# Kernel tuning notes

Hardware: AMD Instinct MI355X
Metric: run time of the kernel (lower is better)

The kernel has to match this reference:

```python
import math
import numpy as np
import jax
import jax.numpy as jnp

B_IN, B_L1, B_L2 = 10, 6, 3
BATCH, NUM_POINTS = 4, 512
F1, F2, F_OUT = 8, 16, 10
NB = BATCH * NUM_POINTS
N_GRID_S2, N_GRID_SO3 = 24, 144


def _lf(n):
    return math.lgamma(n + 1)


def wigner_d(l, beta):
    """Wigner small-d matrices d^l_{m',m}(beta). beta: np [K] -> [K, 2l+1, 2l+1]."""
    beta = np.asarray(beta, dtype=np.float64)
    K = beta.shape[0]
    d = np.zeros((K, 2 * l + 1, 2 * l + 1))
    c, s = np.cos(beta / 2.0), np.sin(beta / 2.0)
    for mi, mp in enumerate(range(-l, l + 1)):
        for ni, m in enumerate(range(-l, l + 1)):
            k0, k1 = max(0, m - mp), min(l + m, l - mp)
            acc = np.zeros(K)
            for k in range(k0, k1 + 1):
                lg = 0.5 * (_lf(l + mp) + _lf(l - mp) + _lf(l + m) + _lf(l - m)) - _lf(l + m - k) - _lf(k) - _lf(mp - m + k) - _lf(l - mp - k)
                acc = acc + ((-1.0) ** (mp - m + k)) * np.exp(lg) * c ** (2 * l - 2 * k + m - mp) * s ** (mp - m + 2 * k)
            d[:, mi, ni] = acc
    return d


def quad_beta_weights(b):
    """Driscoll-Healy quadrature betas and weights at bandwidth b."""
    k = np.arange(2 * b)
    beta = np.pi * (2 * k + 1) / (4 * b)
    j = np.arange(b)[:, None]
    w = (2.0 / b) * np.sin(beta) * np.sum(np.sin((2 * j + 1) * beta[None, :]) / (2 * j + 1), axis=0)
    return beta, w


# near-identity kernel grids (as in s2cnn): s2 grid 3 betas x 8 alphas, so3 grid x 6 gammas
_b = np.arange(1, 4) * (np.pi / 8) / 3
_a = np.linspace(0, 2 * np.pi, 8, endpoint=False)
_GB1, _GA1 = [g.ravel() for g in np.meshgrid(_b, _a, indexing='ij')]
_g = np.linspace(0, 2 * np.pi, 6, endpoint=False)
_GB2, _GA2, _GG2 = [g.ravel() for g in np.meshgrid(_b, _a, _g, indexing='ij')]

_BETA_IN, _W_IN = quad_beta_weights(B_IN)
_BETA_L1, _W_L1 = quad_beta_weights(B_L1)
_BETA_L2, _W_L2 = quad_beta_weights(B_L2)

# S2 FFT tables: quadrature-weighted d^l_{m,0}(beta_k), l < b_l1
_S2FFT_D = [jnp.asarray((wigner_d(l, _BETA_IN)[:, :, l] * _W_IN[:, None]).astype(np.complex64)) for l in range(B_L1)]
# S2 kernel basis psi1[l]: [24, 2l+1] = d^l_{m,0}(beta_g) e^{-i m alpha_g}
_PSI1 = []
for l in range(B_L1):
    m = np.arange(-l, l + 1)
    _PSI1.append(jnp.asarray((wigner_d(l, _GB1)[:, :, l] * np.exp(-1j * m[None, :] * _GA1[:, None])).astype(np.complex64)))
# SO3 inverse-FFT d matrices at b_l1 quadrature betas
_D_L1 = [jnp.asarray(wigner_d(l, _BETA_L1).astype(np.complex64)) for l in range(B_L1)]
# SO3 FFT tables at b_l1 (output bandwidth b_l2)
_SO3FFT_D = [jnp.asarray((wigner_d(l, _BETA_L1) * _W_L1[:, None, None]).astype(np.complex64)) for l in range(B_L2)]
# SO3 kernel basis psi2[l]: [144, 2l+1, 2l+1] = e^{-i m a} d^l_{mn}(b) e^{-i n g}
_PSI2 = []
for l in range(B_L2):
    m = np.arange(-l, l + 1)
    ph = np.exp(-1j * m[None, :, None] * _GA2[:, None, None]) * np.exp(-1j * m[None, None, :] * _GG2[:, None, None])
    _PSI2.append(jnp.asarray((wigner_d(l, _GB2) * ph).astype(np.complex64)))
_D_L2 = [jnp.asarray(wigner_d(l, _BETA_L2).astype(np.complex64)) for l in range(B_L2)]
_W_INT = jnp.asarray(_W_L2.astype(np.float32))


def s2_fft(x, b_out):
    # x: [n, f, 2b(beta), 2b(alpha)] real -> list_l of [n, f, 2l+1] complex
    two_b = x.shape[-1]
    F = jnp.fft.fft(x, axis=-1)
    out = []
    for l in range(b_out):
        idx = np.arange(-l, l + 1) % two_b
        out.append(jnp.einsum('nfkm,km->nfm', F[..., idx], _S2FFT_D[l]))
    return out


def so3_ifft_list(z, b_out, d_list):
    # z[l]: [n, fo, 2l+1(m), 2l+1(p)] -> real [n, fo, 2b(beta), 2b(alpha), 2b(gamma)]
    n2 = 2 * b_out
    n, fo = z[0].shape[:2]
    Fh = jnp.zeros((n, fo, n2, n2, n2), jnp.complex64)
    for l in range(b_out):
        idx = np.arange(-l, l + 1) % n2
        blk = (2 * l + 1) * jnp.einsum('nomp,kmp->nokmp', z[l], d_list[l])
        Fh = Fh.at[:, :, :, idx[:, None], idx[None, :]].add(blk)
    return jnp.real(jnp.fft.ifft2(Fh, axes=(-2, -1)) * (n2 * n2))


def s2_conv(x, w, bias):
    xs = s2_fft(x, B_L1)
    wc = w.astype(jnp.complex64)
    z = []
    for l in range(B_L1):
        y = jnp.einsum('iog,gm->iom', wc, _PSI1[l])  # kernel spectrum [fi, fo, 2l+1]
        z.append(jnp.einsum('nim,iop->nomp', xs[l], jnp.conj(y)))
    return so3_ifft_list(z, B_L1, _D_L1) + bias[None, :, None, None, None]


def so3_fft(x, b_out):
    # x: [n, f, 2b(beta), 2b(alpha), 2b(gamma)] -> list_l of [n, f, 2l+1, 2l+1]
    two_b = x.shape[-1]
    F = jnp.fft.fft2(x, axes=(-2, -1))
    out = []
    for l in range(b_out):
        idx = np.arange(-l, l + 1) % two_b
        out.append(jnp.einsum('nfkmp,kmp->nfmp', F[:, :, :, idx[:, None], idx[None, :]], _SO3FFT_D[l]))
    return out


def so3_conv(x, w, bias):
    xs = so3_fft(x, B_L2)
    wc = w.astype(jnp.complex64)
    z = []
    for l in range(B_L2):
        y = jnp.einsum('iog,gmp->iomp', wc, _PSI2[l])  # [fi, fo, 2l+1, 2l+1]
        z.append(jnp.einsum('nimk,iopk->nomp', xs[l], jnp.conj(y)))
    return so3_ifft_list(z, B_L2, _D_L2) + bias[None, :, None, None, None]


def so3_integrate(x):
    # mean over alpha, gamma; quadrature-weighted sum over beta
    return jnp.einsum('nfk,k->nf', x.mean(axis=(-2, -1)), _W_INT)


def forward(x, w1, b1, w2, b2, w_out, bias_out):
    h = jax.nn.relu(s2_conv(x, w1, b1))
    h = jax.nn.relu(so3_conv(h, w2, b2))
    feat = so3_integrate(h).reshape(BATCH, NUM_POINTS, F2).transpose(0, 2, 1)  # [B, F2, P]
    pooled = feat.max(axis=-1)  # MaxPool1d(kernel_size=num_points) + squeeze
    return pooled @ w_out.T + bias_out


def setup_inputs():
    ks = jax.random.split(jax.random.key(0), 4)
    return {
        'x': jax.random.normal(ks[0], (NB, 1, 2 * B_IN, 2 * B_IN), jnp.float32),
        'w1': jax.random.normal(ks[1], (1, F1, N_GRID_S2), jnp.float32) * 0.1,
        'b1': jnp.zeros((F1,), jnp.float32),
        'w2': jax.random.normal(ks[2], (F1, F2, N_GRID_SO3), jnp.float32) * 0.05,
        'b2': jnp.zeros((F2,), jnp.float32),
        'w_out': jax.random.normal(ks[3], (F_OUT, F2), jnp.float32) * 0.1,
        'bias_out': jnp.zeros((F_OUT,), jnp.float32),
    }


def reference(x, w1, b1, w2, b2, w_out, bias_out):
    return forward(x, w1, b1, w2, b2, w_out, bias_out)
```

## Files before the change

### kernel.cpp

```cpp
#include <hip/hip_runtime.h>
#include <cmath>

typedef float2 c32;

__device__ __forceinline__ void cmadd(c32& acc, c32 a, float cr, float ci){
    acc.x += a.x*cr - a.y*ci;
    acc.y += a.x*ci + a.y*cr;
}

__host__ __device__ constexpr int M12(int x){ return ((x%12)+12)%12; }
__host__ __device__ constexpr int M6(int x){ return ((x%6)+6)%6; }

#define SQ32 0.86602540378443864676f
#define RT22 0.70710678118654752440f
static constexpr float CW12[12] = {1.f, SQ32, 0.5f, 0.f, -0.5f, -SQ32, -1.f, -SQ32, -0.5f, 0.f, 0.5f, SQ32};
static constexpr float SW12[12] = {0.f, 0.5f, SQ32, 1.f, SQ32, 0.5f, 0.f, -0.5f, -SQ32, -1.f, -SQ32, -0.5f};
static constexpr float CW6[6] = {1.f, 0.5f, -0.5f, -1.f, -0.5f, 0.5f};
static constexpr float SW6[6] = {0.f, SQ32, SQ32, 0.f, -SQ32, -SQ32};
static constexpr float CW8[8] = {1.f, RT22, 0.f, -RT22, -1.f, -RT22, 0.f, RT22};
static constexpr float SW8[8] = {0.f, RT22, 1.f, RT22, 0.f, -RT22, -1.f, -RT22};
static constexpr float CW20_[6] = {1.f, 0.95105651629515357212f, 0.80901699437494742410f,
                                   0.58778525229247312917f, 0.30901699437494742410f, 0.f};
static constexpr float SW20_[6] = {0.f, 0.30901699437494742410f, 0.58778525229247312917f,
                                   0.80901699437494742410f, 0.95105651629515357212f, 1.f};

#define O_CY1  0
#define O_CY2P 528
#define O_XS   (O_CY2P + 14080)
#define O_XS2P (O_XS + 73728)
#define N_C32_TOTAL (O_XS2P + 2048*8*30)

#define O_S2D  0
#define O_D1SG 1320
#define O_D2SG 1518
#define O_WINT 1743
#define O_D1S  1752
#define O_DG   (O_D1S + 6336)
#define O_D2P  (O_DG + 360)
#define O_FEAT (O_D2P + 360)

#define DPI 3.14159265358979323846

__device__ __forceinline__ void cell_decode(int c, int& L, int& m, int& p){
    int base;
    if (c < 1){ L=0; base=0; } else if (c < 6){ L=1; base=1; }
    else if (c < 15){ L=2; base=6; } else if (c < 28){ L=3; base=15; }
    else if (c < 45){ L=4; base=28; } else { L=5; base=45; }
    int r = c - base;
    if (r < 2*L){ m = r>>1; p = (r&1)? L : -L; }
    else { m = L; p = (r - 2*L) - L; }
}

static constexpr double FCT[13] = {1.,1.,2.,6.,24.,120.,720.,5040.,40320.,
                                   362880.,3628800.,39916800.,479001600.};

__device__ __forceinline__ double dipow(double b, int e){
    double r = 1.0;
    while (e){ if (e & 1) r *= b; b *= b; e >>= 1; }
    return r;
}

__device__ double dev_wig(int l, int mp, int m, double beta){
    int k0 = max(0, m - mp), k1 = min(l + m, l - mp);
    double c = cos(0.5*beta), s = sin(0.5*beta);
    double fnum = sqrt(FCT[l+mp]*FCT[l-mp]*FCT[l+m]*FCT[l-m]);
    double acc = 0.0;
    for (int k = k0; k <= k1; ++k){
        double t = fnum / (FCT[l+m-k]*FCT[k]*FCT[mp-m+k]*FCT[l-mp-k])
                 * dipow(c, 2*l-2*k+m-mp) * dipow(s, mp-m+2*k);
        acc += ((mp-m+k) & 1) ? -t : t;
    }
    return acc;
}

__device__ double dev_qw(int b, double beta){
    double s = 0.0;
    for (int j = 0; j < b; ++j) s += sin((2.0*j+1.0)*beta)/(2.0*j+1.0);
    return (2.0/b)*sin(beta)*s;
}

__global__ __launch_bounds__(256) void k_setup_pre(float* fb){
    int gid = blockIdx.x*256 + threadIdx.x;
    if (gid < 198){
        int pi = gid%11; int t = gid/11; int ib = t%3; int l = t/3;
        float v = 0.f;
        if (pi < 2*l+1){ double beta = (ib+1)*DPI/24.0; v = (float)dev_wig(l, pi-l, 0, beta); }
        fb[O_D1SG+gid] = v; return;
    }
    gid -= 198;
    if (gid < 225){
        int qi = gid%5; int t = gid/5; int pi = t%5; t /= 5; int ib = t%3; int l = t/3;
        float v = 0.f;
        if (pi < 2*l+1 && qi < 2*l+1){ double beta = (ib+1)*DPI/24.0; v = (float)dev_wig(l, pi-l, qi-l, beta); }
        fb[O_D2SG+gid] = v; return;
    }
    gid -= 225;
    if (gid < 6){ double beta = DPI*(2*gid+1)/12.0; fb[O_WINT+gid] = (float)dev_qw(3, beta); return; }
}

__global__ __launch_bounds__(256) void k_setup_main(c32* cb, float* fb,
                                                    const float* __restrict__ w1,
                                                    const float* __restrict__ w2){
    __shared__ float wsh[144];
    __shared__ c32 W1s[3][8][5];
    __shared__ c32 Rs[3][5][5];
    int bid = blockIdx.x, tid = threadIdx.x;
    if (bid < 128){
        int o = bid >> 3, i = bid & 7;
        for (int c = tid; c < 144; c += 256) wsh[c] = w2[(i*16+o)*144 + c];
        __syncthreads();
        for (int c = tid; c < 120; c += 256){
            int ib = c/40, r = c%40, ia = r/5, qi = r%5;
            int q = qi - 2; int qm = ((q%6)+6)%6;
            float wr = CW6[qm], wi = SW6[qm];
            float er = 1.f, ei = 0.f, sx = 0.f, sy = 0.f;
            const float* wrow = wsh + ib*48 + ia*6;
            #pragma unroll
            for (int ig = 0; ig < 6; ++ig){
                float w = wrow[ig];
                sx += w*er; sy += w*ei;
                float nr = er*wr - ei*wi; ei = er*wi + ei*wr; er = nr;
            }
            W1s[ib][ia][qi] = make_float2(sx, sy);
        }
        __syncthreads();
        for (int c = tid; c < 75; c += 256){
            int ib = c/25, r = c%25, pi = r/5, qi = r%5;
            int p = pi - 2; int pm = ((p%8)+8)%8;
            float wr = CW8[pm], wi = SW8[pm];
            float er = 1.f, ei = 0.f;
            c32 acc = make_float2(0.f,0.f);
            #pragma unroll
            for (int ia = 0; ia < 8; ++ia){
                c32 wv = W1s[ib][ia][qi];
                acc.x += wv.x*er - wv.y*ei;
                acc.y += wv.x*ei + wv.y*er;
                float nr = er*wr - ei*wi; ei = er*wi + ei*wr; er = nr;
            }
            Rs[ib][pi][qi] = acc;
        }
        __syncthreads();
        for (int c = tid; c < 110; c += 256){
            int cell = c/5, qt = c%5;
            int l, p;
            if (cell == 0){ l=0; p=0; }
            else if (cell < 7){ l=1; p=(cell-1)%3 - 1; }
            else { l=2; p=(cell-7)%5 - 2; }
            c32 acc = make_float2(0.f,0.f);
            if (qt < 2*l+1){
                int q = qt - l;
                #pragma unroll
                for (int ib = 0; ib < 3; ++ib){
                    float d = fb[O_D2SG + (l*3+ib)*25 + (p+l)*5 + (q+l)];
                    c32 rv = Rs[ib][p+2][q+2];
                    acc.x += d*rv.x; acc.y += d*rv.y;
                }
            }
            cb[O_CY2P + ((o*22+cell)*8 + i)*5 + qt] = acc;
        }
        return;
    }
    int gid = (bid-128)*256 + tid;
    if (gid < 1320){
        int mi = gid%11; int t = gid/11; int k = t%20; int l = t/20;
        float v = 0.f;
        if (mi < 2*l+1){
            double beta = DPI*(2*k+1)/40.0;
            v = (float)(dev_wig(l, mi-l, 0, beta) * dev_qw(10, beta));
        }
        fb[O_S2D+gid] = v; return;
    }
    gid -= 1320;
    if (gid < 528){
        int pi = gid%11; int t = gid/11; int l = t%6; int o = t/6;
        c32 acc = make_float2(0.f,0.f);
        if (pi < 2*l+1){
            int p = pi - l;
            int pm = ((p%8)+8)%8;
            float wr = CW8[pm], wi = SW8[pm];
            for (int ib = 0; ib < 3; ++ib){
                float d = fb[O_D1SG + (l*3+ib)*11 + pi];
                float er = 1.f, ei = 0.f, sx = 0.f, sy = 0.f;
                #pragma unroll
                for (int ia = 0; ia < 8; ++ia){
                    float w = w1[o*24 + ib*8 + ia];
                    sx += w*er; sy += w*ei;
                    float nr = er*wr - ei*wi; ei = er*wi + ei*wr; er = nr;
                }
                acc.x += d*sx; acc.y += d*sy;
            }
        }
        cb[O_CY1 + (o*6+l)*11 + pi] = acc;
        return;
    }
    gid -= 528;
    if (gid < 6336){
        int k = gid%12; int t = gid/12; int l = t%8; int cell = t/8;
        int L, m, p; cell_decode(cell, L, m, p);
        float v = 0.f;
        if (l < 6 && l >= L){
            double beta = DPI*(2*k+1)/24.0;
            v = (float)dev_wig(l, m, p, beta);
        }
        fb[O_D1S+gid] = v; return;
    }
    gid -= 6336;
    if (gid < 360){
        int k = gid%12; int slot = gid/12;
        int lm = slot/5, qt = slot%5;
        int l = lm==0?0:(lm<3?1:2);
        int m = lm==0?0:(lm<3?lm-1:lm-3);
        float v = 0.f;
        if (qt < 2*l+1){
            double beta = DPI*(2*k+1)/24.0;
            v = (float)(dev_wig(l, m, qt-l, beta) * dev_qw(6, beta));
        }
        fb[O_DG+gid] = v; return;
    }
    gid -= 360;
    if (gid < 360){
        int lp = gid%4; int t = gid/4; int k = t%6; int cell = t/6;
        int m = cell/5, pi = cell%5, p = pi-2, ap = p<0?-p:p;
        float v = 0.f;
        if (lp < 3 && lp >= m && lp >= ap){
            double beta = DPI*(2*k+1)/12.0;
            v = (float)dev_wig(lp, m, p, beta);
        }
        fb[O_D2P+gid] = v; return;
    }
}

__global__ __launch_bounds__(64) void k_s2fft(const float* __restrict__ x, const float* __restrict__ fb,
                                              c32* __restrict__ XS){
    __shared__ float xsh[400];
    __shared__ c32 F1[20][6];
    int n = blockIdx.x, tid = threadIdx.x;
    for (int i = tid; i < 400; i += 64) xsh[i] = x[n*400 + i];
    __syncthreads();
    for (int i = tid; i < 120; i += 64){
        int k = i/6, m = i%6;
        float wr = CW20_[m], wi = -SW20_[m];
        float er = 1.f, ei = 0.f, ax = 0.f, ay = 0.f;
        const float* row = xsh + k*20;
        #pragma unroll
        for (int a = 0; a < 20; ++a){
            float v = row[a];
            ax += v*er; ay += v*ei;
            float nr = er*wr - ei*wi; ei = er*wi + ei*wr; er = nr;
        }
        F1[k][m] = make_float2(ax, ay);
    }
    __syncthreads();
    if (tid < 36){
        int l = 0; while ((l+1)*(l+1) <= tid) ++l;
        int mi = tid - l*l; int m = mi - l;
        c32 acc = make_float2(0.f,0.f);
        for (int k = 0; k < 20; ++k){
            float d = fb[O_S2D + (l*20+k)*11 + mi];
            c32 F = (m >= 0) ? F1[k][m] : make_float2(F1[k][-m].x, -F1[k][-m].y);
            acc.x += d*F.x; acc.y += d*F.y;
        }
        XS[n*36 + tid] = acc;
    }
}

__global__ __launch_bounds__(256) void k_layer1(const c32* __restrict__ cb, const float* __restrict__ fb,
                                                const float* __restrict__ b1, c32* __restrict__ xs2p){
    __shared__ c32 xs_sh[36];
    __shared__ c32 u1[864];
    __shared__ c32 u2[936];
    __shared__ c32 Gg[432];
    __shared__ c32 Gs[180];
    int tid = threadIdx.x;
    int n = blockIdx.x >> 3, o = blockIdx.x & 7;
    float bias = b1[o];
    if (tid < 36) xs_sh[tid] = cb[O_XS + n*36 + tid];
    __syncthreads();

    for (int c = tid; c < 396; c += 256){
        int l = c/66, mp = c - l*66, m = mp/11, pi = mp - m*11;
        int p = pi - 5, ap = p < 0 ? -p : p;
        c32 v = make_float2(0.f, 0.f);
        if (m <= l && ap <= l){
            c32 a = xs_sh[l*l + l + m];
            c32 b = cb[O_CY1 + o*66 + l*11 + p + l];
            float f = (float)(2*l+1);
            v.x = f*(a.x*b.x - a.y*b.y); v.y = f*(a.x*b.y + a.y*b.x);
        }
        u1[c] = v;
    }
    __syncthreads();

    if (tid < 132){
        int cell = tid >> 1, kh = tid & 1;
        int L, m, p; cell_decode(cell, L, m, p);
        int mp = m*11 + p + 5;
        c32 acc[6];
        #pragma unroll
        for (int j = 0; j < 6; ++j) acc[j] = make_float2(0.f,0.f);
        for (int l = L; l < 6; ++l){
            c32 z = u1[l*66 + mp];
            const float* dp = fb + O_D1S + (cell*8 + l)*12 + kh*6;
            #pragma unroll
            for (int j = 0; j < 6; ++j){
                float d = dp[j];
                acc[j].x += d*z.x; acc[j].y += d*z.y;
            }
        }
        #pragma unroll
        for (int j = 0; j < 6; ++j) u2[mp*12 + kh*6 + j] = acc[j];
    }
    __syncthreads();

    if (tid < 72){
        int m = tid/12, k = tid - m*12;
        c32 S0 = u2[(m*11+5)*12 + k];
        c32 E[5], O[5];
        #pragma unroll
        for (int p = 1; p <= 5; ++p){
            c32 a = u2[(m*11+5+p)*12 + k], b = u2[(m*11+5-p)*12 + k];
            E[p-1] = make_float2(a.x+b.x, a.y+b.y);
            O[p-1] = make_float2(a.x-b.x, a.y-b.y);
        }
        #pragma unroll
        for (int g = 0; g < 6; ++g){
            float vex=0.f, vey=0.f, vox=0.f, voy=0.f;
            #pragma unroll
            for (int p = 1; p <= 5; ++p){
                const float cc = CW12[M12(p*g)], ss = SW12[M12(p*g)];
                float vx = E[p-1].x*cc - O[p-1].y*ss;
                float vy = E[p-1].y*cc + O[p-1].x*ss;
                if (p & 1){ vox += vx; voy += vy; } else { vex += vx; vey += vy; }
            }
            float tex = S0.x + vex, tey = S0.y + vey;
            u1[(m*12+g)*12 + k]   = make_float2(tex + vox, tey + voy);
            u1[(m*12+g+6)*12 + k] = make_float2(tex - vox, tey - voy);
        }
    }
    __syncthreads();

    float* hh = (float*)u2;
    if (tid < 144){
        int g = tid/12, k = tid - g*12;
        c32 t1 = u1[(1*12+g)*12+k], t2 = u1[(2*12+g)*12+k], t3 = u1[(3*12+g)*12+k];
        c32 t4 = u1[(4*12+g)*12+k], t5 = u1[(5*12+g)*12+k];
        float base = u1[(0*12+g)*12+k].x + bias;
        #pragma unroll
        for (int a = 0; a < 6; ++a){
            float od = t1.x*CW12[M12(1*a)] - t1.y*SW12[M12(1*a)]
                     + t3.x*CW12[M12(3*a)] - t3.y*SW12[M12(3*a)]
                     + t5.x*CW12[M12(5*a)] - t5.y*SW12[M12(5*a)];
            float ev = t2.x*CW12[M12(2*a)] - t2.y*SW12[M12(2*a)]
                     + t4.x*CW12[M12(4*a)] - t4.y*SW12[M12(4*a)];
            float h0 = base + 2.f*(ev+od);
            float h1 = base + 2.f*(ev-od);
            hh[(g*12+a)*13+k]     = h0 > 0.f ? h0 : 0.f;
            hh[(g*12+a+6)*13+k]   = h1 > 0.f ? h1 : 0.f;
        }
    }
    __syncthreads();

    if (tid < 144){
        int a = tid/12, k = tid - a*12;
        float hv[12];
        #pragma unroll
        for (int g = 0; g < 12; ++g) hv[g] = hh[(g*12+a)*13+k];
        float s0 = 0.f;
        #pragma unroll
        for (int g = 0; g < 12; ++g) s0 += hv[g];
        Gg[a*12+k] = make_float2(s0, 0.f);
        #pragma unroll
        for (int mg = 1; mg < 3; ++mg){
            float ax = 0.f, ay = 0.f;
            #pragma unroll
            for (int g = 0; g < 12; ++g){
                const int tt = M12(mg*g);
                ax += hv[g]*CW12[tt]; ay -= hv[g]*SW12[tt];
            }
            Gg[(mg*12+a)*12+k] = make_float2(ax, ay);
        }
    }
    __syncthreads();

    if (tid < 108){
        int j = tid/36, r = tid - j*36, mg = r/12, k = r - mg*12;
        const c32* gp = Gg + mg*144 + k;
        if (j == 0){
            float sx = 0.f, sy = 0.f;
            #pragma unroll
            for (int a = 0; a < 6; ++a){
                c32 xa = gp[a*12], ya = gp[(a+6)*12];
                sx += xa.x + ya.x; sy += xa.y + ya.y;
            }
            Gs[(2*3+mg)*12+k] = make_float2(sx, sy);
        } else if (j == 1){
            float Cx=0.f,Cy=0.f,Sx=0.f,Sy=0.f;
            #pragma unroll
            for (int a = 0; a < 6; ++a){
                c32 xa = gp[a*12], ya = gp[(a+6)*12];
                float ux = xa.x - ya.x, uy = xa.y - ya.y;
                const float cc = CW12[a], ss = SW12[a];
                Cx += ux*cc; Cy += uy*cc;
                Sx += ux*ss; Sy += uy*ss;
            }
            Gs[(3*3+mg)*12+k] = make_float2(Cx + Sy, Cy - Sx);
            Gs[(1*3+mg)*12+k] = make_float2(Cx - Sy, Cy + Sx);
        } else {
            float Cx=0.f,Cy=0.f,Sx=0.f,Sy=0.f;
            #pragma unroll
            for (int a = 0; a < 6; ++a){
                c32 xa = gp[a*12], ya = gp[(a+6)*12];
                float ux = xa.x + ya.x, uy = xa.y + ya.y;
                const float cc = CW12[M12(2*a)], ss = SW12[M12(2*a)];
                Cx += ux*cc; Cy += uy*cc;
                Sx += ux*ss; Sy += uy*ss;
            }
            Gs[(4*3+mg)*12+k] = make_float2(Cx + Sy, Cy - Sx);
            Gs[(0*3+mg)*12+k] = make_float2(Cx - Sy, Cy + Sx);
        }
    }
    __syncthreads();

    if (tid < 30){
        int lm = tid/5, qt = tid - lm*5;
        int l = lm==0?0:(lm<3?1:2);
        int m = lm==0?0:(lm<3?lm-1:lm-3);
        c32 acc = make_float2(0.f,0.f);
        if (qt < 2*l+1){
            int q = qt - l;
            #pragma unroll
            for (int k = 0; k < 12; ++k){
                float d = fb[O_DG + tid*12 + k];
                c32 gvv;
                if (q >= 0) gvv = Gs[((m+2)*3 + q)*12 + k];
                else { c32 w = Gs[((2-m)*3 + (-q))*12 + k]; gvv = make_float2(w.x, -w.y); }
                acc.x += d*gvv.x; acc.y += d*gvv.y;
            }
        }
        xs2p[(n*8+o)*30 + tid] = acc;
    }
}

__global__ __launch_bounds__(256) void k_layer2(const c32* __restrict__ cb, const float* __restrict__ fb,
                                                const float* __restrict__ b2, float* __restrict__ feat){
    __shared__ c32 xs2sh[960];
    __shared__ c32 zp2[4][384];
    __shared__ c32 T2[1728];
    __shared__ float part[576];
    int tid = threadIdx.x, n0 = blockIdx.x*4;
    for (int c = tid; c < 960; c += 256) xs2sh[c] = cb[O_XS2P + n0*240 + c];
    __syncthreads();

    for (int c = tid; c < 1408; c += 256){
        int nl = c/352, cc = c - nl*352, o = cc/22, cell = cc - o*22;
        int l, lm;
        if (cell == 0){ l=0; lm=0; }
        else if (cell < 7){ l=1; lm=1+(cell-1)/3; }
        else { l=2; lm=3+(cell-7)/5; }
        const c32* cy = cb + O_CY2P + (o*22+cell)*40;
        const c32* xv0 = xs2sh + nl*240;
        c32 acc = make_float2(0.f,0.f);
        #pragma unroll
        for (int i = 0; i < 8; ++i){
            #pragma unroll
            for (int qt = 0; qt < 5; ++qt){
                c32 xv = xv0[(i*6+lm)*5 + qt];
                c32 yv = cy[i*5+qt];
                acc.x += xv.x*yv.x - xv.y*yv.y;
                acc.y += xv.x*yv.y + xv.y*yv.x;
            }
        }
        float f = (float)(2*l+1);
        zp2[nl][o*24+cell] = make_float2(f*acc.x, f*acc.y);
    }
    __syncthreads();

    for (int nl = 0; nl < 4; ++nl){
        for (int c = tid; c < 288; c += 256){
            int o = c/18, r = c - o*18, k = r/3, m = r - k*3;
            c32 s2v[5];
            #pragma unroll
            for (int pi = 0; pi < 5; ++pi){
                const int p = pi-2; const int ap = p<0?-p:p;
                c32 acc = make_float2(0.f,0.f);
                #pragma unroll
                for (int l = 0; l < 3; ++l){
                    if (l >= ap){
                        float d = fb[O_D2P + ((m*5+pi)*6+k)*4 + l];
                        int cell = (l==0) ? 0 : ((l==1) ? 1+m*3+(p+1) : 7+m*5+(p+2));
                        c32 z = zp2[nl][o*24+cell];
                        acc.x += d*z.x; acc.y += d*z.y;
                    }
                }
                s2v[pi] = acc;
            }
            #pragma unroll
            for (int g = 0; g < 6; ++g){
                c32 t = make_float2(0.f,0.f);
                #pragma unroll
                for (int pi = 0; pi < 5; ++pi){
                    const int tt = M6((pi-2)*g);
                    cmadd(t, s2v[pi], CW6[tt], SW6[tt]);
                }
                T2[((o*6+k)*3+m)*6+g] = t;
            }
        }
        __syncthreads();
        for (int c = tid; c < 576; c += 256){
            int o = c/36, r = c - o*36, k = r/6, g = r - k*6;
            c32 t0 = T2[((o*6+k)*3+0)*6+g];
            c32 t1 = T2[((o*6+k)*3+1)*6+g];
            c32 t2 = T2[((o*6+k)*3+2)*6+g];
            float base = t0.x + b2[o];
            float s = 0.f;
            #pragma unroll
            for (int a = 0; a < 6; ++a){
                float h = base + 2.f*(t1.x*CW6[M6(a)]   - t1.y*SW6[M6(a)])
                               + 2.f*(t2.x*CW6[M6(2*a)] - t2.y*SW6[M6(2*a)]);
                s += h > 0.f ? h : 0.f;
            }
            part[c] = s * fb[O_WINT + k];
        }
        __syncthreads();
        if (tid < 16){
            float s = 0.f;
            #pragma unroll
            for (int j = 0; j < 36; ++j) s += part[tid*36+j];
            feat[(n0+nl)*16+tid] = s * (1.f/36.f);
        }
        __syncthreads();
    }
}

__global__ __launch_bounds__(256) void k_poolhead(const float* __restrict__ feat,
                                                  const float* __restrict__ w_out,
                                                  const float* __restrict__ bias_out,
                                                  float* __restrict__ out){
    __shared__ float red[256];
    __shared__ float pool_s[64];
    int tid = threadIdx.x;
    int pair = tid >> 2, chunk = tid & 3;
    int b = pair >> 4, o = pair & 15;
    float m = -3.4e38f;
    for (int j = 0; j < 128; ++j){
        int pt = chunk*128 + j;
        m = fmaxf(m, feat[(b*512+pt)*16 + o]);
    }
    red[tid] = m;
    __syncthreads();
    if (tid < 64){
        pool_s[tid] = fmaxf(fmaxf(red[tid*4], red[tid*4+1]),
                            fmaxf(red[tid*4+2], red[tid*4+3]));
    }
    __syncthreads();
    if (tid < 40){
        int bb = tid/10, jj = tid%10;
        float s = bias_out[jj];
        #pragma unroll
        for (int oo = 0; oo < 16; ++oo) s += pool_s[bb*16+oo]*w_out[jj*16+oo];
        out[tid] = s;
    }
}

extern "C" void kernel_launch(void* const* d_in, const int* in_sizes, int n_in,
                              void* d_out, int out_size, void* d_ws, size_t ws_size,
                              hipStream_t stream){
    const float* x        = (const float*)d_in[0];
    const float* w1       = (const float*)d_in[1];
    const float* b1       = (const float*)d_in[2];
    const float* w2       = (const float*)d_in[3];
    const float* b2       = (const float*)d_in[4];
    const float* w_out    = (const float*)d_in[5];
    const float* bias_out = (const float*)d_in[6];
    float* out = (float*)d_out;

    c32*   cb = (c32*)d_ws;
    float* fb = (float*)(cb + N_C32_TOTAL);
    float* feat = fb + O_FEAT;

    k_setup_pre<<<2, 256, 0, stream>>>(fb);
    k_setup_main<<<163, 256, 0, stream>>>(cb, fb, w1, w2);
    k_s2fft<<<2048, 64, 0, stream>>>(x, fb, cb + O_XS);
    k_layer1<<<2048*8, 256, 0, stream>>>(cb, fb, b1, cb + O_XS2P);
    k_layer2<<<512, 256, 0, stream>>>(cb, fb, b2, feat);
    k_poolhead<<<1, 256, 0, stream>>>(feat, w_out, bias_out, out);
}
```

Measured before the change: 198.7 us.

## Merge setup kernels, batch s2fft per block, split pool/head, reuse cy across points

Folds the small pre-setup kernel into the main setup kernel by computing Wigner tables in shared memory or inline, which removes one launch. The S2 FFT kernel now handles four points per 256-thread block instead of one per 64-thread block. Layer2 reuses each cy coefficient load across four points, and the quadrature weights are computed in shared memory. The single-block pool/head kernel is split into a 64-block parallel max reduction using wave shuffles plus a tiny head kernel, which adds a launch in exchange for more parallelism.

```diff
diff --git a/kernel.cpp b/kernel.cpp
--- a/kernel.cpp
+++ b/kernel.cpp
@@ -31,13 +31,11 @@
 #define N_C32_TOTAL (O_XS2P + 2048*8*30)
 
 #define O_S2D  0
-#define O_D1SG 1320
-#define O_D2SG 1518
-#define O_WINT 1743
 #define O_D1S  1752
 #define O_DG   (O_D1S + 6336)
 #define O_D2P  (O_DG + 360)
 #define O_FEAT (O_D2P + 360)
+#define O_POOL (O_FEAT + 32768)
 
 #define DPI 3.14159265358979323846
 
@@ -79,35 +77,23 @@
     return (2.0/b)*sin(beta)*s;
 }
 
-__global__ __launch_bounds__(256) void k_setup_pre(float* fb){
-    int gid = blockIdx.x*256 + threadIdx.x;
-    if (gid < 198){
-        int pi = gid%11; int t = gid/11; int ib = t%3; int l = t/3;
-        float v = 0.f;
-        if (pi < 2*l+1){ double beta = (ib+1)*DPI/24.0; v = (float)dev_wig(l, pi-l, 0, beta); }
-        fb[O_D1SG+gid] = v; return;
-    }
-    gid -= 198;
-    if (gid < 225){
-        int qi = gid%5; int t = gid/5; int pi = t%5; t /= 5; int ib = t%3; int l = t/3;
-        float v = 0.f;
-        if (pi < 2*l+1 && qi < 2*l+1){ double beta = (ib+1)*DPI/24.0; v = (float)dev_wig(l, pi-l, qi-l, beta); }
-        fb[O_D2SG+gid] = v; return;
-    }
-    gid -= 225;
-    if (gid < 6){ double beta = DPI*(2*gid+1)/12.0; fb[O_WINT+gid] = (float)dev_qw(3, beta); return; }
-}
-
-__global__ __launch_bounds__(256) void k_setup_main(c32* cb, float* fb,
-                                                    const float* __restrict__ w1,
-                                                    const float* __restrict__ w2){
+__global__ __launch_bounds__(256) void k_setup(c32* cb, float* fb,
+                                               const float* __restrict__ w1,
+                                               const float* __restrict__ w2){
     __shared__ float wsh[144];
+    __shared__ float s_d2sg[225];
     __shared__ c32 W1s[3][8][5];
     __shared__ c32 Rs[3][5][5];
     int bid = blockIdx.x, tid = threadIdx.x;
     if (bid < 128){
         int o = bid >> 3, i = bid & 7;
         for (int c = tid; c < 144; c += 256) wsh[c] = w2[(i*16+o)*144 + c];
+        for (int c = tid; c < 225; c += 256){
+            int qi = c%5; int t = c/5; int pi = t%5; t /= 5; int ib = t%3; int l = t/3;
+            float v = 0.f;
+            if (pi < 2*l+1 && qi < 2*l+1){ double beta = (ib+1)*DPI/24.0; v = (float)dev_wig(l, pi-l, qi-l, beta); }
+            s_d2sg[c] = v;
+        }
         __syncthreads();
         for (int c = tid; c < 120; c += 256){
             int ib = c/40, r = c%40, ia = r/5, qi = r%5;
@@ -151,7 +137,7 @@
                 int q = qt - l;
                 #pragma unroll
                 for (int ib = 0; ib < 3; ++ib){
-                    float d = fb[O_D2SG + (l*3+ib)*25 + (p+l)*5 + (q+l)];
+                    float d = s_d2sg[(l*3+ib)*25 + (p+l)*5 + (q+l)];
                     c32 rv = Rs[ib][p+2][q+2];
                     acc.x += d*rv.x; acc.y += d*rv.y;
                 }
@@ -179,7 +165,7 @@
             int pm = ((p%8)+8)%8;
             float wr = CW8[pm], wi = SW8[pm];
             for (int ib = 0; ib < 3; ++ib){
-                float d = fb[O_D1SG + (l*3+ib)*11 + pi];
+                float d = (float)dev_wig(l, pi-l, 0, (ib+1)*DPI/24.0);
                 float er = 1.f, ei = 0.f, sx = 0.f, sy = 0.f;
                 #pragma unroll
                 for (int ia = 0; ia < 8; ++ia){
@@ -230,37 +216,38 @@
     }
 }
 
-__global__ __launch_bounds__(64) void k_s2fft(const float* __restrict__ x, const float* __restrict__ fb,
-                                              c32* __restrict__ XS){
-    __shared__ float xsh[400];
-    __shared__ c32 F1[20][6];
-    int n = blockIdx.x, tid = threadIdx.x;
-    for (int i = tid; i < 400; i += 64) xsh[i] = x[n*400 + i];
-    __syncthreads();
-    for (int i = tid; i < 120; i += 64){
-        int k = i/6, m = i%6;
+__global__ __launch_bounds__(256) void k_s2fft(const float* __restrict__ x, const float* __restrict__ fb,
+                                               c32* __restrict__ XS){
+    __shared__ float xsh[1600];
+    __shared__ c32 F1[4][20][6];
+    int n0 = blockIdx.x*4, tid = threadIdx.x;
+    for (int i = tid; i < 1600; i += 256) xsh[i] = x[n0*400 + i];
+    __syncthreads();
+    for (int i = tid; i < 480; i += 256){
+        int nl = i/120, r = i - nl*120, k = r/6, m = r - k*6;
         float wr = CW20_[m], wi = -SW20_[m];
         float er = 1.f, ei = 0.f, ax = 0.f, ay = 0.f;
-        const float* row = xsh + k*20;
+        const float* row = xsh + nl*400 + k*20;
         #pragma unroll
         for (int a = 0; a < 20; ++a){
             float v = row[a];
             ax += v*er; ay += v*ei;
             float nr = er*wr - ei*wi; ei = er*wi + ei*wr; er = nr;
         }
-        F1[k][m] = make_float2(ax, ay);
-    }
-    __syncthreads();
-    if (tid < 36){
-        int l = 0; while ((l+1)*(l+1) <= tid) ++l;
-        int mi = tid - l*l; int m = mi - l;
+        F1[nl][k][m] = make_float2(ax, ay);
+    }
+    __syncthreads();
+    if (tid < 144){
+        int nl = tid/36, t = tid - nl*36;
+        int l = 0; while ((l+1)*(l+1) <= t) ++l;
+        int mi = t - l*l; int m = mi - l;
         c32 acc = make_float2(0.f,0.f);
         for (int k = 0; k < 20; ++k){
             float d = fb[O_S2D + (l*20+k)*11 + mi];
-            c32 F = (m >= 0) ? F1[k][m] : make_float2(F1[k][-m].x, -F1[k][-m].y);
+            c32 F = (m >= 0) ? F1[nl][k][m] : make_float2(F1[nl][k][-m].x, -F1[nl][k][-m].y);
             acc.x += d*F.x; acc.y += d*F.y;
         }
-        XS[n*36 + tid] = acc;
+        XS[(n0+nl)*36 + t] = acc;
     }
 }
 
@@ -383,7 +370,7 @@
     __syncthreads();
 
     if (tid < 108){
-        int j = tid/36, r = tid - j*36, mg = r/12, k = r - mg*12;
+        int j = tid/36, rr = tid - j*36, mg = rr/12, k = rr - mg*12;
         const c32* gp = Gg + mg*144 + k;
         if (j == 0){
             float sx = 0.f, sy = 0.f;
@@ -447,31 +434,39 @@
     __shared__ c32 zp2[4][384];
     __shared__ c32 T2[1728];
     __shared__ float part[576];
+    __shared__ float wint_sh[6];
     int tid = threadIdx.x, n0 = blockIdx.x*4;
     for (int c = tid; c < 960; c += 256) xs2sh[c] = cb[O_XS2P + n0*240 + c];
-    __syncthreads();
-
-    for (int c = tid; c < 1408; c += 256){
-        int nl = c/352, cc = c - nl*352, o = cc/22, cell = cc - o*22;
+    if (tid < 6){ double beta = DPI*(2*tid+1)/12.0; wint_sh[tid] = (float)dev_qw(3, beta); }
+    __syncthreads();
+
+    for (int c = tid; c < 352; c += 256){
+        int o = c/22, cell = c - o*22;
         int l, lm;
         if (cell == 0){ l=0; lm=0; }
         else if (cell < 7){ l=1; lm=1+(cell-1)/3; }
         else { l=2; lm=3+(cell-7)/5; }
         const c32* cy = cb + O_CY2P + (o*22+cell)*40;
-        const c32* xv0 = xs2sh + nl*240;
-        c32 acc = make_float2(0.f,0.f);
+        c32 acc[4];
+        #pragma unroll
+        for (int nl = 0; nl < 4; ++nl) acc[nl] = make_float2(0.f,0.f);
         #pragma unroll
         for (int i = 0; i < 8; ++i){
             #pragma unroll
             for (int qt = 0; qt < 5; ++qt){
-                c32 xv = xv0[(i*6+lm)*5 + qt];
                 c32 yv = cy[i*5+qt];
-                acc.x += xv.x*yv.x - xv.y*yv.y;
-                acc.y += xv.x*yv.y + xv.y*yv.x;
+                #pragma unroll
+                for (int nl = 0; nl < 4; ++nl){
+                    c32 xv = xs2sh[nl*240 + (i*6+lm)*5 + qt];
+                    acc[nl].x += xv.x*yv.x - xv.y*yv.y;
+                    acc[nl].y += xv.x*yv.y + xv.y*yv.x;
+                }
             }
         }
         float f = (float)(2*l+1);
-        zp2[nl][o*24+cell] = make_float2(f*acc.x, f*acc.y);
+        #pragma unroll
+        for (int nl = 0; nl < 4; ++nl)
+            zp2[nl][o*24+cell] = make_float2(f*acc[nl].x, f*acc[nl].y);
     }
     __syncthreads();
 
@@ -519,7 +514,7 @@
                                + 2.f*(t2.x*CW6[M6(2*a)] - t2.y*SW6[M6(2*a)]);
                 s += h > 0.f ? h : 0.f;
             }
-            part[c] = s * fb[O_WINT + k];
+            part[c] = s * wint_sh[k];
         }
         __syncthreads();
         if (tid < 16){
@@ -532,32 +527,23 @@
     }
 }
 
-__global__ __launch_bounds__(256) void k_poolhead(const float* __restrict__ feat,
-                                                  const float* __restrict__ w_out,
-                                                  const float* __restrict__ bias_out,
-                                                  float* __restrict__ out){
-    __shared__ float red[256];
-    __shared__ float pool_s[64];
+__global__ __launch_bounds__(64) void k_pool(const float* __restrict__ feat, float* __restrict__ pool){
+    int b = blockIdx.x >> 4, o = blockIdx.x & 15;
     int tid = threadIdx.x;
-    int pair = tid >> 2, chunk = tid & 3;
-    int b = pair >> 4, o = pair & 15;
     float m = -3.4e38f;
-    for (int j = 0; j < 128; ++j){
-        int pt = chunk*128 + j;
+    for (int pt = tid; pt < 512; pt += 64)
         m = fmaxf(m, feat[(b*512+pt)*16 + o]);
-    }
-    red[tid] = m;
-    __syncthreads();
-    if (tid < 64){
-        pool_s[tid] = fmaxf(fmaxf(red[tid*4], red[tid*4+1]),
-                            fmaxf(red[tid*4+2], red[tid*4+3]));
-    }
-    __syncthreads();
+    for (int off = 32; off; off >>= 1) m = fmaxf(m, __shfl_down(m, off));
+    if (tid == 0) pool[b*16 + o] = m;
+}
+
+__global__ __launch_bounds__(64) void k_head(const float* __restrict__ pool, const float* __restrict__ w_out,
+                                             const float* __restrict__ bias_out, float* __restrict__ out){
+    int tid = threadIdx.x;
     if (tid < 40){
-        int bb = tid/10, jj = tid%10;
-        float s = bias_out[jj];
-        #pragma unroll
-        for (int oo = 0; oo < 16; ++oo) s += pool_s[bb*16+oo]*w_out[jj*16+oo];
+        int b = tid/10, j = tid%10;
+        float s = bias_out[j];
+        for (int o = 0; o < 16; ++o) s += pool[b*16+o]*w_out[j*16+o];
         out[tid] = s;
     }
 }
@@ -577,11 +563,12 @@
     c32*   cb = (c32*)d_ws;
     float* fb = (float*)(cb + N_C32_TOTAL);
     float* feat = fb + O_FEAT;
-
-    k_setup_pre<<<2, 256, 0, stream>>>(fb);
-    k_setup_main<<<163, 256, 0, stream>>>(cb, fb, w1, w2);
-    k_s2fft<<<2048, 64, 0, stream>>>(x, fb, cb + O_XS);
+    float* pool = fb + O_POOL;
+
+    k_setup<<<163, 256, 0, stream>>>(cb, fb, w1, w2);
+    k_s2fft<<<512, 256, 0, stream>>>(x, fb, cb + O_XS);
     k_layer1<<<2048*8, 256, 0, stream>>>(cb, fb, b1, cb + O_XS2P);
     k_layer2<<<512, 256, 0, stream>>>(cb, fb, b2, feat);
-    k_poolhead<<<1, 256, 0, stream>>>(feat, w_out, bias_out, out);
-}
+    k_pool<<<64, 64, 0, stream>>>(feat, pool);
+    k_head<<<1, 64, 0, stream>>>(pool, w_out, bias_out, out);
+}
```

Result: faster. 172.3 us (-13.3%).
